# Kernel optimization log

Hardware: AMD Instinct MI355X
Metric: run time of the kernel (lower is better)

Reference implementation:

```python
import jax, jax.numpy as jnp
import numpy as np

D_MODEL = 2048
N_HEADS = 32
N_KV_HEADS = 8
HEAD_DIM = D_MODEL // N_HEADS  # 64
ROPE_THETA = 10000.0


def _build_rope_cache(seq_len, head_dim, theta):
    half = head_dim // 2
    inv_freq = 1.0 / theta ** (jnp.arange(half, dtype=jnp.float32) / half)
    pos = jnp.arange(seq_len, dtype=jnp.float32)
    freqs = jnp.outer(pos, inv_freq)  # [S, half]
    return jnp.cos(freqs), jnp.sin(freqs)


def _apply_rope(x, cos, sin):
    # x: [B, H, S, D]; cos/sin: [S, D//2] -> broadcast [1,1,S,D//2]
    x_even = x[..., ::2]
    x_odd = x[..., 1::2]
    c = cos[None, None]
    s = sin[None, None]
    rot_even = x_even * c - x_odd * s
    rot_odd = x_even * s + x_odd * c
    # interleave back: stack on last axis then flatten
    return jnp.stack((rot_even, rot_odd), axis=-1).reshape(x.shape)


def setup_inputs() -> dict:
    key = jax.random.key(0)
    k0, k1, k2, k3, k4 = jax.random.split(key, 5)
    B, S = 2, 2048
    scale = 0.02
    x = jax.random.normal(k0, (B, S, D_MODEL), dtype=jnp.float32)
    Wq = jax.random.normal(k1, (D_MODEL, N_HEADS * HEAD_DIM), dtype=jnp.float32) * scale
    Wk = jax.random.normal(k2, (D_MODEL, N_KV_HEADS * HEAD_DIM), dtype=jnp.float32) * scale
    Wv = jax.random.normal(k3, (D_MODEL, N_KV_HEADS * HEAD_DIM), dtype=jnp.float32) * scale
    Wo = jax.random.normal(k4, (D_MODEL, D_MODEL), dtype=jnp.float32) * scale
    return {"x": x, "Wq": Wq, "Wk": Wk, "Wv": Wv, "Wo": Wo}


def reference(x, Wq, Wk, Wv, Wo):
    B, S, _ = x.shape
    q = (x @ Wq).reshape(B, S, N_HEADS, HEAD_DIM).transpose(0, 2, 1, 3)      # [B,H,S,D]
    k = (x @ Wk).reshape(B, S, N_KV_HEADS, HEAD_DIM).transpose(0, 2, 1, 3)   # [B,Hk,S,D]
    v = (x @ Wv).reshape(B, S, N_KV_HEADS, HEAD_DIM).transpose(0, 2, 1, 3)
    cos, sin = _build_rope_cache(S, HEAD_DIM, ROPE_THETA)
    q = _apply_rope(q, cos, sin)
    k = _apply_rope(k, cos, sin)
    repeat = N_HEADS // N_KV_HEADS
    if repeat > 1:
        k = jnp.repeat(k, repeat, axis=1)
        v = jnp.repeat(v, repeat, axis=1)
    scores = jnp.einsum("bhqd,bhkd->bhqk", q, k) / jnp.sqrt(jnp.float32(HEAD_DIM))
    causal = jnp.tril(jnp.ones((S, S), dtype=bool))
    neg = -jnp.finfo(scores.dtype).max
    scores = jnp.where(causal[None, None], scores, neg)
    probs = jax.nn.softmax(scores.astype(jnp.float32), axis=-1).astype(x.dtype)
    out = jnp.einsum("bhqk,bhkd->bhqd", probs, v)
    out = out.transpose(0, 2, 1, 3).reshape(B, S, D_MODEL)
    return out @ Wo
```

## Files before the change

### kernel.cpp

```cpp
#include <hip/hip_runtime.h>
#include <cstdint>

typedef unsigned short u16;
typedef __attribute__((ext_vector_type(8))) __bf16 bf16x8;
typedef __attribute__((ext_vector_type(4))) float f32x4;

#define S_LEN 2048

__device__ __forceinline__ u16 f2bf(float f) {
  uint32_t u = __builtin_bit_cast(uint32_t, f);
  u += 0x7fffu + ((u >> 16) & 1u);
  return (u16)(u >> 16);
}
__device__ __forceinline__ float bf2f(u16 h) {
  return __builtin_bit_cast(float, (uint32_t)h << 16);
}
__device__ __forceinline__ bf16x8 ldfrag(const u16* p) {
  return __builtin_bit_cast(bf16x8, *(const uint4*)p);
}
__device__ __forceinline__ f32x4 mfma16(bf16x8 a, bf16x8 b, f32x4 c) {
  return __builtin_amdgcn_mfma_f32_16x16x32_bf16(a, b, c, 0, 0, 0);
}
__device__ __forceinline__ void glds16(const u16* g, u16* l) {
  __builtin_amdgcn_global_load_lds((const __attribute__((address_space(1))) void*)g,
                                   (__attribute__((address_space(3))) void*)l, 16, 0, 0);
}

__global__ __launch_bounds__(256) void cvt_kernel(const float* __restrict__ in,
                                                  u16* __restrict__ out, int n4) {
  int i = blockIdx.x * 256 + threadIdx.x;
  if (i >= n4) return;
  float4 v = ((const float4*)in)[i];
  ushort4 o;
  o.x = f2bf(v.x); o.y = f2bf(v.y); o.z = f2bf(v.z); o.w = f2bf(v.w);
  ((ushort4*)out)[i] = o;
}

__global__ __launch_bounds__(256) void cvtT_kernel(const float* __restrict__ W,
                                                   u16* __restrict__ Wt, int K, int N) {
  __shared__ float t[32][33];
  int tx = threadIdx.x & 31, ty = threadIdx.x >> 5;
  int n0 = blockIdx.x * 32, k0 = blockIdx.y * 32;
#pragma unroll
  for (int j = 0; j < 4; ++j)
    t[ty + 8 * j][tx] = W[(long)(k0 + ty + 8 * j) * N + n0 + tx];
  __syncthreads();
#pragma unroll
  for (int j = 0; j < 4; ++j)
    Wt[(long)(n0 + ty + 8 * j) * K + k0 + tx] = f2bf(t[tx][ty + 8 * j]);
}

template <int MODE>
__global__ __launch_bounds__(256) void gemm_bt(const u16* __restrict__ A,
                                               const u16* __restrict__ Bt,
                                               void* __restrict__ C, int K, int ldc) {
  __shared__ __align__(16) u16 As[128 * 32];
  __shared__ __align__(16) u16 Bs[128 * 32];
  int tid = threadIdx.x;
  int lane = tid & 63, w = tid >> 6;
  int wr = (w >> 1) * 64, wc = (w & 1) * 64;
  int l15 = lane & 15, l4 = lane >> 4;
  int rowbase = blockIdx.x * 128, colbase = blockIdx.y * 128;
  f32x4 acc[4][4] = {};
  int r0 = tid >> 2, kc0 = (tid & 3) * 8;
  const u16* Ap0 = A + (long)(rowbase + r0) * K + kc0;
  const u16* Ap1 = A + (long)(rowbase + 64 + r0) * K + kc0;
  const u16* Bp0 = Bt + (long)(colbase + r0) * K + kc0;
  const u16* Bp1 = Bt + (long)(colbase + 64 + r0) * K + kc0;
  u16* Asl0 = As + w * 512;
  u16* Asl1 = As + 2048 + w * 512;
  u16* Bsl0 = Bs + w * 512;
  u16* Bsl1 = Bs + 2048 + w * 512;
  for (int k0 = 0; k0 < K; k0 += 32) {
    __syncthreads();
    glds16(Ap0 + k0, Asl0);
    glds16(Ap1 + k0, Asl1);
    glds16(Bp0 + k0, Bsl0);
    glds16(Bp1 + k0, Bsl1);
    __syncthreads();
    bf16x8 af[4], bv[4];
#pragma unroll
    for (int m = 0; m < 4; ++m) af[m] = ldfrag(&As[(wr + m * 16 + l15) * 32 + l4 * 8]);
#pragma unroll
    for (int n = 0; n < 4; ++n) bv[n] = ldfrag(&Bs[(wc + n * 16 + l15) * 32 + l4 * 8]);
#pragma unroll
    for (int m = 0; m < 4; ++m)
#pragma unroll
      for (int n = 0; n < 4; ++n) acc[m][n] = mfma16(af[m], bv[n], acc[m][n]);
  }
#pragma unroll
  for (int m = 0; m < 4; ++m)
#pragma unroll
    for (int n = 0; n < 4; ++n) {
      if (MODE == 2) {
        int row = rowbase + wr + m * 16 + l4 * 4;
        int col = colbase + wc + n * 16 + l15;
        int b_ = row >> 11, s_ = row & 2047;
        int kvh_ = col >> 6, d_ = col & 63;
        ushort4 pk;
        pk.x = f2bf(acc[m][n][0]); pk.y = f2bf(acc[m][n][1]);
        pk.z = f2bf(acc[m][n][2]); pk.w = f2bf(acc[m][n][3]);
        *(ushort4*)&((u16*)C)[((long)((b_ * 8 + kvh_) * 64 + d_)) * 2048 + s_] = pk;
      } else {
#pragma unroll
        for (int r = 0; r < 4; ++r) {
          int row = rowbase + wr + m * 16 + l4 * 4 + r;
          int col = colbase + wc + n * 16 + l15;
          if (MODE == 1)
            ((u16*)C)[(long)row * ldc + col] = f2bf(acc[m][n][r]);
          else
            ((float*)C)[(long)row * ldc + col] = acc[m][n][r];
        }
      }
    }
}

__global__ __launch_bounds__(256) void rope_tab_kernel(float2* __restrict__ ctab) {
  int idx = blockIdx.x * 256 + threadIdx.x;
  int i = idx & 31, s = idx >> 5;
  float freq = exp2f(-(float)i * (13.287712379549449f / 32.0f));
  float sn, cs;
  sincosf((float)s * freq, &sn, &cs);
  ctab[idx] = make_float2(cs, sn);
}

__global__ __launch_bounds__(256) void kpack_kernel(const u16* __restrict__ Ks,
                                                    const float2* __restrict__ ctab,
                                                    u16* __restrict__ Kp) {
  int idx = blockIdx.x * 256 + threadIdx.x;
  int lane = idx & 63, half = (idx >> 6) & 1, n = (idx >> 7) & 3;
  int t = (idx >> 9) & 31, kvh = (idx >> 14) & 7, b = idx >> 17;
  int l15 = lane & 15, l4 = lane >> 4;
  int s = t * 64 + n * 16 + l15;
  int d0 = half * 32 + l4 * 8;
  const u16* src = Ks + ((long)(b * 2048 + s)) * 512 + kvh * 64 + d0;
  uint4 v = *(const uint4*)src;
  const float2* ct = ctab + s * 32 + (d0 >> 1);
  uint32_t o[4];
#pragma unroll
  for (int jj = 0; jj < 4; ++jj) {
    uint32_t vw = ((const uint32_t*)&v)[jj];
    float2 cs = ct[jj];
    float e = bf2f((u16)vw), od = bf2f((u16)(vw >> 16));
    float re = e * cs.x - od * cs.y;
    float ro = e * cs.y + od * cs.x;
    o[jj] = (uint32_t)f2bf(re) | ((uint32_t)f2bf(ro) << 16);
  }
  *(uint4*)(Kp + (long)idx * 8) = *(uint4*)o;
}

__global__ __launch_bounds__(256) void vpack_kernel(const u16* __restrict__ Vt,
                                                    u16* __restrict__ Vp) {
  int idx = blockIdx.x * 256 + threadIdx.x;
  int lane = idx & 63, half = (idx >> 6) & 1, f = (idx >> 7) & 3;
  int t = (idx >> 9) & 31, kvh = (idx >> 14) & 7, b = idx >> 17;
  int l15 = lane & 15, l4 = lane >> 4;
  const u16* src = Vt + ((long)((b * 8 + kvh) * 64 + f * 16 + l15)) * 2048 +
                   t * 64 + half * 32 + l4 * 8;
  *(uint4*)(Vp + (long)idx * 8) = *(const uint4*)src;
}

__global__ __launch_bounds__(256, 8) void attn_kernel(const u16* __restrict__ Q,
                                                      const u16* __restrict__ Kp,
                                                      const u16* __restrict__ Vp,
                                                      const float2* __restrict__ ctab,
                                                      u16* __restrict__ O) {
  int bid = blockIdx.x;
  int p = bid & 31, h = (bid >> 5) & 31, b = bid >> 10;
  int kvh = h >> 2;
  int tid = threadIdx.x, lane = tid & 63, w = tid >> 6;
  int l15 = lane & 15, l4 = lane >> 4;
  int cc = (w + p) & 3;
  int c = cc == 0 ? 2 * p : cc == 1 ? 2 * p + 1 : cc == 2 ? 127 - 2 * p : 126 - 2 * p;
  int qb = c * 16;
  int nt = (c >> 2) + 1;
  __shared__ u16 Ps[4][16][72];
  u16(*myPs)[72] = Ps[w];
  const u16* Qh = Q + (long)b * S_LEN * 2048 + h * 64;
  const u16* Kh = Kp + (long)(b * 8 + kvh) * 131072;
  const u16* Vh = Vp + (long)(b * 8 + kvh) * 131072;
  u16* Oh = O + (long)b * S_LEN * 2048 + h * 64;
  int s = qb + l15;
  const u16* qp = Qh + (long)s * 2048;
  uint4 r0 = *(const uint4*)(qp + l4 * 8);
  uint4 r1 = *(const uint4*)(qp + 32 + l4 * 8);
  const float2* ct = ctab + (long)s * 32 + l4 * 4;
  uint32_t q0w[4], q1w[4];
#pragma unroll
  for (int jj = 0; jj < 4; ++jj) {
    float2 cs0 = ct[jj], cs1 = ct[16 + jj];
    uint32_t v0 = ((const uint32_t*)&r0)[jj], v1 = ((const uint32_t*)&r1)[jj];
    float e0 = bf2f((u16)v0), o0 = bf2f((u16)(v0 >> 16));
    float e1 = bf2f((u16)v1), o1 = bf2f((u16)(v1 >> 16));
    float a0 = (e0 * cs0.x - o0 * cs0.y) * 0.125f;
    float b0 = (e0 * cs0.y + o0 * cs0.x) * 0.125f;
    float a1 = (e1 * cs1.x - o1 * cs1.y) * 0.125f;
    float b1 = (e1 * cs1.y + o1 * cs1.x) * 0.125f;
    q0w[jj] = (uint32_t)f2bf(a0) | ((uint32_t)f2bf(b0) << 16);
    q1w[jj] = (uint32_t)f2bf(a1) | ((uint32_t)f2bf(b1) << 16);
  }
  bf16x8 qf0 = __builtin_bit_cast(bf16x8, *(uint4*)q0w);
  bf16x8 qf1 = __builtin_bit_cast(bf16x8, *(uint4*)q1w);
  float m_r = -INFINITY, l_r = 0.f;
  f32x4 oaccT[4] = {};
  int lane8 = lane * 8;
  for (int t = 0; t < nt; ++t) {
    const u16* kt = Kh + t * 4096;
    f32x4 sacc[4] = {};
#pragma unroll
    for (int n = 0; n < 4; ++n) {
      sacc[n] = mfma16(ldfrag(kt + n * 1024 + lane8), qf0, sacc[n]);
      sacc[n] = mfma16(ldfrag(kt + n * 1024 + 512 + lane8), qf1, sacc[n]);
    }
    if (t == nt - 1) {
      int kb = t * 64;
#pragma unroll
      for (int n = 0; n < 4; ++n) {
        int kc_ = kb + n * 16 + l4 * 4;
#pragma unroll
        for (int r = 0; r < 4; ++r)
          if (kc_ + r > qb + l15) sacc[n][r] = -1e30f;
      }
    }
    float mx = fmaxf(fmaxf(fmaxf(sacc[0][0], sacc[0][1]), fmaxf(sacc[0][2], sacc[0][3])),
                     fmaxf(fmaxf(sacc[1][0], sacc[1][1]), fmaxf(sacc[1][2], sacc[1][3])));
    mx = fmaxf(mx, fmaxf(fmaxf(fmaxf(sacc[2][0], sacc[2][1]), fmaxf(sacc[2][2], sacc[2][3])),
                         fmaxf(fmaxf(sacc[3][0], sacc[3][1]), fmaxf(sacc[3][2], sacc[3][3]))));
    mx = fmaxf(mx, __shfl_xor(mx, 16));
    mx = fmaxf(mx, __shfl_xor(mx, 32));
    float mn = fmaxf(m_r, mx);
    float fac = __expf(m_r - mn);
    m_r = mn;
    float rs = 0.f;
#pragma unroll
    for (int n = 0; n < 4; ++n) {
      float p0 = __expf(sacc[n][0] - mn);
      float p1 = __expf(sacc[n][1] - mn);
      float p2 = __expf(sacc[n][2] - mn);
      float p3 = __expf(sacc[n][3] - mn);
      rs += (p0 + p1) + (p2 + p3);
      ushort4 pk;
      pk.x = f2bf(p0); pk.y = f2bf(p1); pk.z = f2bf(p2); pk.w = f2bf(p3);
      *(ushort4*)&myPs[l15][n * 16 + l4 * 4] = pk;
    }
    rs += __shfl_xor(rs, 16);
    rs += __shfl_xor(rs, 32);
    l_r = l_r * fac + rs;
#pragma unroll
    for (int f = 0; f < 4; ++f) {
      oaccT[f][0] *= fac; oaccT[f][1] *= fac;
      oaccT[f][2] *= fac; oaccT[f][3] *= fac;
    }
    bf16x8 pa0 = ldfrag(&myPs[l15][l4 * 8]);
    bf16x8 pa1 = ldfrag(&myPs[l15][32 + l4 * 8]);
    const u16* vt = Vh + t * 4096;
#pragma unroll
    for (int f = 0; f < 4; ++f) {
      oaccT[f] = mfma16(ldfrag(vt + f * 1024 + lane8), pa0, oaccT[f]);
      oaccT[f] = mfma16(ldfrag(vt + f * 1024 + 512 + lane8), pa1, oaccT[f]);
    }
  }
  float linv = 1.f / l_r;
#pragma unroll
  for (int f = 0; f < 4; ++f) {
    ushort4 pk;
    pk.x = f2bf(oaccT[f][0] * linv); pk.y = f2bf(oaccT[f][1] * linv);
    pk.z = f2bf(oaccT[f][2] * linv); pk.w = f2bf(oaccT[f][3] * linv);
    *(ushort4*)&Oh[(long)(qb + l15) * 2048 + f * 16 + l4 * 4] = pk;
  }
}

extern "C" void kernel_launch(void* const* d_in, const int* in_sizes, int n_in,
                              void* d_out, int out_size, void* d_ws, size_t ws_size,
                              hipStream_t stream) {
  const float* x = (const float*)d_in[0];
  const float* Wq = (const float*)d_in[1];
  const float* Wk = (const float*)d_in[2];
  const float* Wv = (const float*)d_in[3];
  const float* Wo = (const float*)d_in[4];
  float* out = (float*)d_out;
  char* ws = (char*)d_ws;
  u16* xb = (u16*)(ws + 0);
  u16* WqT = (u16*)(ws + 16777216);
  u16* WkT = (u16*)(ws + 25165824);
  u16* WvT = (u16*)(ws + 27262976);
  u16* WoT = (u16*)(ws + 29360128);
  u16* Qs = (u16*)(ws + 37748736);
  u16* Ks = (u16*)(ws + 54525952);
  u16* Vt = (u16*)(ws + 58720256);
  u16* Os = (u16*)(ws + 62914560);
  u16* Kp = (u16*)(ws + 16777216);
  u16* Vp = (u16*)(ws + 20971520);
  float2* ctab = (float2*)(ws + 79691776);

  cvt_kernel<<<8192, 256, 0, stream>>>(x, xb, 2097152);
  cvtT_kernel<<<dim3(64, 64), 256, 0, stream>>>(Wq, WqT, 2048, 2048);
  cvtT_kernel<<<dim3(16, 64), 256, 0, stream>>>(Wk, WkT, 2048, 512);
  cvtT_kernel<<<dim3(16, 64), 256, 0, stream>>>(Wv, WvT, 2048, 512);
  cvtT_kernel<<<dim3(64, 64), 256, 0, stream>>>(Wo, WoT, 2048, 2048);
  rope_tab_kernel<<<256, 256, 0, stream>>>(ctab);
  gemm_bt<1><<<dim3(32, 16), 256, 0, stream>>>(xb, WqT, Qs, 2048, 2048);
  gemm_bt<1><<<dim3(32, 4), 256, 0, stream>>>(xb, WkT, Ks, 2048, 512);
  gemm_bt<2><<<dim3(32, 4), 256, 0, stream>>>(xb, WvT, Vt, 2048, 512);
  kpack_kernel<<<1024, 256, 0, stream>>>(Ks, ctab, Kp);
  vpack_kernel<<<1024, 256, 0, stream>>>(Vt, Vp);
  attn_kernel<<<2048, 256, 0, stream>>>(Qs, Kp, Vp, ctab, Os);
  gemm_bt<0><<<dim3(32, 16), 256, 0, stream>>>(Os, WoT, out, 2048, 2048);
}
```

Baseline: 452.0 us.

## Fuse QKV projections into one GEMM and triple-buffer LDS loads

Merges the three Q/K/V projection GEMMs into a single launch over a concatenated transposed weight. Each block routes its output tile to Q, K or transposed V according to its column range. The GEMM main loop now uses a three-stage LDS ring, issuing global-to-LDS loads two tiles ahead with explicit vmcnt waits and one barrier per iteration instead of two. This is meant to hide load latency and cut launch overhead and tail effects, at the cost of three times the LDS use, which may lower occupancy. The Kp/Vp workspace offsets were moved so they do not overlap the fused weight buffer, which would still be live while they are written.

```diff
diff --git a/kernel.cpp b/kernel.cpp
--- a/kernel.cpp
+++ b/kernel.cpp
@@ -53,9 +53,11 @@
 template <int MODE>
 __global__ __launch_bounds__(256) void gemm_bt(const u16* __restrict__ A,
                                                const u16* __restrict__ Bt,
-                                               void* __restrict__ C, int K, int ldc) {
-  __shared__ __align__(16) u16 As[128 * 32];
-  __shared__ __align__(16) u16 Bs[128 * 32];
+                                               void* __restrict__ C, int K, int ldc,
+                                               u16* __restrict__ Kc_out,
+                                               u16* __restrict__ Vt_out) {
+  __shared__ __align__(16) u16 As[3][4096];
+  __shared__ __align__(16) u16 Bs[3][4096];
   int tid = threadIdx.x;
   int lane = tid & 63, w = tid >> 6;
   int wr = (w >> 1) * 64, wc = (w & 1) * 64;
@@ -67,52 +69,91 @@
   const u16* Ap1 = A + (long)(rowbase + 64 + r0) * K + kc0;
   const u16* Bp0 = Bt + (long)(colbase + r0) * K + kc0;
   const u16* Bp1 = Bt + (long)(colbase + 64 + r0) * K + kc0;
-  u16* Asl0 = As + w * 512;
-  u16* Asl1 = As + 2048 + w * 512;
-  u16* Bsl0 = Bs + w * 512;
-  u16* Bsl1 = Bs + 2048 + w * 512;
-  for (int k0 = 0; k0 < K; k0 += 32) {
-    __syncthreads();
-    glds16(Ap0 + k0, Asl0);
-    glds16(Ap1 + k0, Asl1);
-    glds16(Bp0 + k0, Bsl0);
-    glds16(Bp1 + k0, Bsl1);
-    __syncthreads();
+  int wb = w * 512;
+  auto stage = [&](int t, int buf) {
+    int ko = t * 32;
+    glds16(Ap0 + ko, &As[buf][wb]);
+    glds16(Ap1 + ko, &As[buf][2048 + wb]);
+    glds16(Bp0 + ko, &Bs[buf][wb]);
+    glds16(Bp1 + ko, &Bs[buf][2048 + wb]);
+  };
+  int nk = K >> 5;
+  stage(0, 0);
+  stage(1, 1);
+  asm volatile("s_waitcnt vmcnt(4)" ::: "memory");
+  __builtin_amdgcn_s_barrier();
+  int cur = 0, nxt2 = 2;
+  for (int t = 0; t < nk; ++t) {
+    if (t + 2 < nk) stage(t + 2, nxt2);
     bf16x8 af[4], bv[4];
 #pragma unroll
-    for (int m = 0; m < 4; ++m) af[m] = ldfrag(&As[(wr + m * 16 + l15) * 32 + l4 * 8]);
-#pragma unroll
-    for (int n = 0; n < 4; ++n) bv[n] = ldfrag(&Bs[(wc + n * 16 + l15) * 32 + l4 * 8]);
+    for (int m = 0; m < 4; ++m) af[m] = ldfrag(&As[cur][(wr + m * 16 + l15) * 32 + l4 * 8]);
+#pragma unroll
+    for (int n = 0; n < 4; ++n) bv[n] = ldfrag(&Bs[cur][(wc + n * 16 + l15) * 32 + l4 * 8]);
 #pragma unroll
     for (int m = 0; m < 4; ++m)
 #pragma unroll
       for (int n = 0; n < 4; ++n) acc[m][n] = mfma16(af[m], bv[n], acc[m][n]);
-  }
-#pragma unroll
-  for (int m = 0; m < 4; ++m)
-#pragma unroll
-    for (int n = 0; n < 4; ++n) {
-      if (MODE == 2) {
-        int row = rowbase + wr + m * 16 + l4 * 4;
-        int col = colbase + wc + n * 16 + l15;
-        int b_ = row >> 11, s_ = row & 2047;
-        int kvh_ = col >> 6, d_ = col & 63;
-        ushort4 pk;
-        pk.x = f2bf(acc[m][n][0]); pk.y = f2bf(acc[m][n][1]);
-        pk.z = f2bf(acc[m][n][2]); pk.w = f2bf(acc[m][n][3]);
-        *(ushort4*)&((u16*)C)[((long)((b_ * 8 + kvh_) * 64 + d_)) * 2048 + s_] = pk;
-      } else {
+    if (t + 1 < nk) {
+      if (t + 2 < nk)
+        asm volatile("s_waitcnt vmcnt(4)" ::: "memory");
+      else
+        asm volatile("s_waitcnt vmcnt(0)" ::: "memory");
+      __builtin_amdgcn_s_barrier();
+    }
+    cur = cur == 2 ? 0 : cur + 1;
+    nxt2 = nxt2 == 2 ? 0 : nxt2 + 1;
+  }
+  if (MODE == 0) {
+#pragma unroll
+    for (int m = 0; m < 4; ++m)
+#pragma unroll
+      for (int n = 0; n < 4; ++n)
 #pragma unroll
         for (int r = 0; r < 4; ++r) {
           int row = rowbase + wr + m * 16 + l4 * 4 + r;
           int col = colbase + wc + n * 16 + l15;
-          if (MODE == 1)
-            ((u16*)C)[(long)row * ldc + col] = f2bf(acc[m][n][r]);
-          else
-            ((float*)C)[(long)row * ldc + col] = acc[m][n][r];
+          ((float*)C)[(long)row * ldc + col] = acc[m][n][r];
         }
-      }
-    }
+  } else {
+    if (colbase < 2048) {
+#pragma unroll
+      for (int m = 0; m < 4; ++m)
+#pragma unroll
+        for (int n = 0; n < 4; ++n)
+#pragma unroll
+          for (int r = 0; r < 4; ++r) {
+            int row = rowbase + wr + m * 16 + l4 * 4 + r;
+            int col = colbase + wc + n * 16 + l15;
+            ((u16*)C)[(long)row * 2048 + col] = f2bf(acc[m][n][r]);
+          }
+    } else if (colbase < 2560) {
+#pragma unroll
+      for (int m = 0; m < 4; ++m)
+#pragma unroll
+        for (int n = 0; n < 4; ++n)
+#pragma unroll
+          for (int r = 0; r < 4; ++r) {
+            int row = rowbase + wr + m * 16 + l4 * 4 + r;
+            int col = colbase + wc + n * 16 + l15 - 2048;
+            Kc_out[(long)row * 512 + col] = f2bf(acc[m][n][r]);
+          }
+    } else {
+#pragma unroll
+      for (int m = 0; m < 4; ++m)
+#pragma unroll
+        for (int n = 0; n < 4; ++n) {
+          int row = rowbase + wr + m * 16 + l4 * 4;
+          int col = colbase + wc + n * 16 + l15 - 2560;
+          int b_ = row >> 11, s_ = row & 2047;
+          int kvh_ = col >> 6, d_ = col & 63;
+          ushort4 pk;
+          pk.x = f2bf(acc[m][n][0]); pk.y = f2bf(acc[m][n][1]);
+          pk.z = f2bf(acc[m][n][2]); pk.w = f2bf(acc[m][n][3]);
+          *(ushort4*)&Vt_out[((long)((b_ * 8 + kvh_) * 64 + d_)) * 2048 + s_] = pk;
+        }
+    }
+  }
 }
 
 __global__ __launch_bounds__(256) void rope_tab_kernel(float2* __restrict__ ctab) {
@@ -281,29 +322,25 @@
   float* out = (float*)d_out;
   char* ws = (char*)d_ws;
   u16* xb = (u16*)(ws + 0);
-  u16* WqT = (u16*)(ws + 16777216);
-  u16* WkT = (u16*)(ws + 25165824);
-  u16* WvT = (u16*)(ws + 27262976);
+  u16* WqkvT = (u16*)(ws + 16777216);
   u16* WoT = (u16*)(ws + 29360128);
   u16* Qs = (u16*)(ws + 37748736);
   u16* Ks = (u16*)(ws + 54525952);
   u16* Vt = (u16*)(ws + 58720256);
   u16* Os = (u16*)(ws + 62914560);
-  u16* Kp = (u16*)(ws + 16777216);
-  u16* Vp = (u16*)(ws + 20971520);
+  u16* Kp = (u16*)(ws + 0);
+  u16* Vp = (u16*)(ws + 4194304);
   float2* ctab = (float2*)(ws + 79691776);
 
   cvt_kernel<<<8192, 256, 0, stream>>>(x, xb, 2097152);
-  cvtT_kernel<<<dim3(64, 64), 256, 0, stream>>>(Wq, WqT, 2048, 2048);
-  cvtT_kernel<<<dim3(16, 64), 256, 0, stream>>>(Wk, WkT, 2048, 512);
-  cvtT_kernel<<<dim3(16, 64), 256, 0, stream>>>(Wv, WvT, 2048, 512);
+  cvtT_kernel<<<dim3(64, 64), 256, 0, stream>>>(Wq, WqkvT, 2048, 2048);
+  cvtT_kernel<<<dim3(16, 64), 256, 0, stream>>>(Wk, WqkvT + 4194304, 2048, 512);
+  cvtT_kernel<<<dim3(16, 64), 256, 0, stream>>>(Wv, WqkvT + 5242880, 2048, 512);
   cvtT_kernel<<<dim3(64, 64), 256, 0, stream>>>(Wo, WoT, 2048, 2048);
   rope_tab_kernel<<<256, 256, 0, stream>>>(ctab);
-  gemm_bt<1><<<dim3(32, 16), 256, 0, stream>>>(xb, WqT, Qs, 2048, 2048);
-  gemm_bt<1><<<dim3(32, 4), 256, 0, stream>>>(xb, WkT, Ks, 2048, 512);
-  gemm_bt<2><<<dim3(32, 4), 256, 0, stream>>>(xb, WvT, Vt, 2048, 512);
+  gemm_bt<3><<<dim3(32, 24), 256, 0, stream>>>(xb, WqkvT, Qs, 2048, 2048, Ks, Vt);
   kpack_kernel<<<1024, 256, 0, stream>>>(Ks, ctab, Kp);
   vpack_kernel<<<1024, 256, 0, stream>>>(Vt, Vp);
   attn_kernel<<<2048, 256, 0, stream>>>(Qs, Kp, Vp, ctab, Os);
-  gemm_bt<0><<<dim3(32, 16), 256, 0, stream>>>(Os, WoT, out, 2048, 2048);
-}
+  gemm_bt<0><<<dim3(32, 16), 256, 0, stream>>>(Os, WoT, out, 2048, 2048, nullptr, nullptr);
+}
```

New measurement: 369.3 us. -18.3%, faster.
